# Kernel optimization log

Hardware: AMD Instinct MI355X
Metric: run time of the kernel (lower is better)

The kernel has to match this reference:

```python
import jax, jax.numpy as jnp
import numpy as np
from math import sqrt

H = 16
D_MODEL = 1024
D_K = D_MODEL // H
B, S = 2, 2048


def setup_inputs() -> dict:
    key = jax.random.key(0)
    ks = jax.random.split(key, 12)
    scale = 1.0 / sqrt(D_MODEL)
    inp = {
        "query": jax.random.normal(ks[0], (B, S, D_MODEL), jnp.float32),
        "key": jax.random.normal(ks[1], (B, S, D_MODEL), jnp.float32),
        "value": jax.random.normal(ks[2], (B, S, D_MODEL), jnp.float32),
        # causal mask [B, S, S]; module unsqueezes head dim itself
        "mask": jnp.broadcast_to(jnp.tril(jnp.ones((S, S), jnp.int32)), (B, S, S)),
        "Wq": jax.random.normal(ks[3], (D_MODEL, D_MODEL), jnp.float32) * scale,
        "bq": jnp.zeros((D_MODEL,), jnp.float32),
        "Wk": jax.random.normal(ks[4], (D_MODEL, D_MODEL), jnp.float32) * scale,
        "bk": jnp.zeros((D_MODEL,), jnp.float32),
        "Wv": jax.random.normal(ks[5], (D_MODEL, D_MODEL), jnp.float32) * scale,
        "bv": jnp.zeros((D_MODEL,), jnp.float32),
        "Wo": jax.random.normal(ks[6], (D_MODEL, D_MODEL), jnp.float32) * scale,
        "bo": jnp.zeros((D_MODEL,), jnp.float32),
    }
    return inp


def reference(query, key, value, mask, Wq, bq, Wk, bk, Wv, bv, Wo, bo):
    nb = query.shape[0]

    def proj(x, W, b):
        # nn.Linear: x @ W.T + b, then split heads -> [B, H, S, D_K]
        y = jnp.einsum('bsd,ed->bse', x, W) + b
        return y.reshape(nb, -1, H, D_K).transpose(0, 2, 1, 3)

    q = proj(query, Wq, bq)
    k = proj(key, Wk, bk)
    v = proj(value, Wv, bv)

    scores = jnp.einsum('bhqd,bhkd->bhqk', q, k) / sqrt(D_K)  # [B,H,S,S]
    scores = jnp.where(mask[:, None, :, :] == 0, -jnp.inf, scores)
    probs = jax.nn.softmax(scores, axis=-1)  # dropout in eval mode (identity)
    ctx = jnp.einsum('bhqk,bhkd->bhqd', probs, v)
    ctx = ctx.transpose(0, 2, 1, 3).reshape(nb, -1, H * D_K)
    return jnp.einsum('bsd,ed->bse', ctx, Wo) + bo
```

## Files before the change

kernel.cpp:

```cpp
#include <hip/hip_runtime.h>
#include <hip/hip_bf16.h>
#include <stdint.h>


#define H_ 16
#define DM 1024
#define DK_ 64
#define BB 2
#define SS 2048
#define PSTR 72

typedef __bf16 bf16x8 __attribute__((ext_vector_type(8)));
typedef __bf16 bf16x2_t __attribute__((ext_vector_type(2)));
typedef float f32x4 __attribute__((ext_vector_type(4)));

#define GLOAD_LDS16(g, l)                                            \
  __builtin_amdgcn_global_load_lds(                                  \
      (__attribute__((address_space(1))) void*)(g),                  \
      (__attribute__((address_space(3))) void*)(l), 16, 0, 0)

__device__ __forceinline__ unsigned short f2bf_u(float f) {
  unsigned int u = __float_as_uint(f);
  u += 0x7fffu + ((u >> 16) & 1u);
  return (unsigned short)(u >> 16);
}

__device__ __forceinline__ unsigned int pack_bf16(float a, float b) {
#if __has_builtin(__builtin_amdgcn_cvt_pk_bf16_f32)
  bf16x2_t v = __builtin_amdgcn_cvt_pk_bf16_f32(a, b);
  unsigned int u;
  __builtin_memcpy(&u, &v, 4);
  return u;
#else
  return (unsigned int)f2bf_u(a) | ((unsigned int)f2bf_u(b) << 16);
#endif
}

__device__ __forceinline__ float fexp2(float x) {
#if __has_builtin(__builtin_amdgcn_exp2f)
  return __builtin_amdgcn_exp2f(x);
#else
  return exp2f(x);
#endif
}

struct Cvt {
  const float* s[7];
  unsigned short* d[7];
  int n[7];
};

__global__ __launch_bounds__(256) void convert_kernel(Cvt c) {
  const int y = blockIdx.y;
  const float* __restrict__ src = c.s[y];
  unsigned short* __restrict__ dst = c.d[y];
  const int nv = c.n[y] >> 2;
  for (int i = blockIdx.x * 256 + threadIdx.x; i < nv; i += 1024 * 256) {
    float4 v = *(const float4*)(src + (size_t)i * 4);
    ushort4 o;
    o.x = f2bf_u(v.x); o.y = f2bf_u(v.y); o.z = f2bf_u(v.z); o.w = f2bf_u(v.w);
    *(ushort4*)(dst + (size_t)i * 4) = o;
  }
}

template <int TN>
__device__ __forceinline__ void gemm_dbuf(
    const unsigned short* __restrict__ A, const unsigned short* __restrict__ W,
    unsigned short* As, unsigned short* Bs, int m0, int n0,
    f32x4 (*acc)[TN / 32]) {
  constexpr int FW = TN / 32;
  const int tid = threadIdx.x;
  const int wave = tid >> 6, lane = tid & 63;
  const int lm = lane & 15, quad = lane >> 4;
  const int wm = (wave >> 1) * 64, wn = (wave & 1) * (16 * FW);
  const int srow = lane >> 2;
  const int scol = (lane & 3) * 8;

#pragma unroll
  for (int i = 0; i < 4; ++i)
#pragma unroll
    for (int j = 0; j < FW; ++j) {
      f32x4 z = {0.f, 0.f, 0.f, 0.f};
      acc[i][j] = z;
    }

#pragma unroll
  for (int cc = 0; cc < 2; ++cc) {
    int c = wave * 2 + cc;
    GLOAD_LDS16(A + (size_t)(m0 + c * 16 + srow) * DM + scol,
                As + c * 512 + lane * 8);
  }
  if (TN == 128) {
#pragma unroll
    for (int cc = 0; cc < 2; ++cc) {
      int c = wave * 2 + cc;
      GLOAD_LDS16(W + (size_t)(n0 + c * 16 + srow) * DM + scol,
                  Bs + c * 512 + lane * 8);
    }
  } else {
    GLOAD_LDS16(W + (size_t)(n0 + wave * 16 + srow) * DM + scol,
                Bs + wave * 512 + lane * 8);
  }

  for (int kt = 0; kt < DM / 32; ++kt) {
    __syncthreads();
    const int cur = kt & 1;
    const unsigned short* Ac = As + cur * (128 * 32);
    const unsigned short* Bc = Bs + cur * (TN * 32);
    if (kt + 1 < DM / 32) {
      unsigned short* An = As + (cur ^ 1) * (128 * 32);
      unsigned short* Bn = Bs + (cur ^ 1) * (TN * 32);
      const int kcol = (kt + 1) * 32 + scol;
#pragma unroll
      for (int cc = 0; cc < 2; ++cc) {
        int c = wave * 2 + cc;
        GLOAD_LDS16(A + (size_t)(m0 + c * 16 + srow) * DM + kcol,
                    An + c * 512 + lane * 8);
      }
      if (TN == 128) {
#pragma unroll
        for (int cc = 0; cc < 2; ++cc) {
          int c = wave * 2 + cc;
          GLOAD_LDS16(W + (size_t)(n0 + c * 16 + srow) * DM + kcol,
                      Bn + c * 512 + lane * 8);
        }
      } else {
        GLOAD_LDS16(W + (size_t)(n0 + wave * 16 + srow) * DM + kcol,
                    Bn + wave * 512 + lane * 8);
      }
    }
    bf16x8 af[4], bfr[FW];
#pragma unroll
    for (int i = 0; i < 4; ++i)
      af[i] = *(const bf16x8*)(Ac + (wm + i * 16 + lm) * 32 + quad * 8);
#pragma unroll
    for (int j = 0; j < FW; ++j)
      bfr[j] = *(const bf16x8*)(Bc + (wn + j * 16 + lm) * 32 + quad * 8);
#pragma unroll
    for (int i = 0; i < 4; ++i)
#pragma unroll
      for (int j = 0; j < FW; ++j)
        acc[i][j] = __builtin_amdgcn_mfma_f32_16x16x32_bf16(af[i], bfr[j],
                                                            acc[i][j], 0, 0, 0);
  }
}

__global__ __launch_bounds__(512, 2) void qkv_gemm(
    const unsigned short* Qi, const unsigned short* Ki, const unsigned short* Vi,
    const unsigned short* Wq, const unsigned short* Wk, const unsigned short* Wv,
    const float* bq, const float* bk, const float* bv,
    unsigned short* Qf, unsigned short* Kf, unsigned short* Vf) {
  __shared__ unsigned short As[2 * 2 * 16 * 512];
  __shared__ unsigned short Bs[2 * 2 * 16 * 512];
  const int p = blockIdx.x;
  const int c = p & 7, idx = p >> 3;
  const int x = idx & 3, yy = (idx >> 2) & 1, z = idx >> 3;
  const int y = c * 2 + yy;
  const int m0 = y * 256, n0 = x * 256;
  const unsigned short* A = z == 0 ? Qi : (z == 1 ? Ki : Vi);
  const unsigned short* W = z == 0 ? Wq : (z == 1 ? Wk : Wv);
  const float* bias = z == 0 ? bq : (z == 1 ? bk : bv);
  const float scale = z == 0 ? 0.125f : 1.0f;

  const int tid = threadIdx.x;
  const int wave = tid >> 6, lane = tid & 63;
  const int lm = lane & 15, quad = lane >> 4;
  const int wr = wave >> 2, wc = wave & 3;

  const int scs = 8 * ((lane & 3) ^ ((lane >> 3) & 3));
  const size_t asrc0 = (size_t)(m0 + wave * 16 + (lane >> 2)) * DM + scs;
  const size_t bsrc0 = (size_t)(n0 + wave * 16 + (lane >> 2)) * DM + scs;
  const int sdst = wave * 512 + lane * 8;

  const int rcol = (quad * 8) ^ (((lm >> 1) & 3) * 8);
  const int aoff = wr * 8 * 512 + lm * 32 + rcol;
  const int boff = wc * 4 * 512 + lm * 32 + rcol;

  f32x4 acc[8][4];
#pragma unroll
  for (int i = 0; i < 8; ++i)
#pragma unroll
    for (int j = 0; j < 4; ++j) {
      f32x4 zz = {0.f, 0.f, 0.f, 0.f};
      acc[i][j] = zz;
    }

  auto stA = [&](int buf, int kh, int kt) {
    const unsigned short* s = A + asrc0 + (size_t)kt * 64 + kh * 32;
    unsigned short* d = As + buf * 16384 + kh * 8192 + sdst;
    GLOAD_LDS16(s, d);
    GLOAD_LDS16(s + (size_t)128 * DM, d + 4096);
  };
  auto stB = [&](int buf, int kh, int kt) {
    const unsigned short* s = W + bsrc0 + (size_t)kt * 64 + kh * 32;
    unsigned short* d = Bs + buf * 16384 + kh * 8192 + sdst;
    GLOAD_LDS16(s, d);
    GLOAD_LDS16(s + (size_t)128 * DM, d + 4096);
  };

  stA(0, 0, 0); stB(0, 0, 0); stA(0, 1, 0); stB(0, 1, 0);
  stA(1, 0, 1); stB(1, 0, 1); stA(1, 1, 1);
  asm volatile("s_waitcnt vmcnt(6)" ::: "memory");
  __builtin_amdgcn_s_barrier();

#define BARR __builtin_amdgcn_s_barrier()
#define SCHB __builtin_amdgcn_sched_barrier(0)
#define MFMA8(AF, B0_, B1_, J0, J1)                                          \
  __builtin_amdgcn_s_setprio(1);                                             \
  _Pragma("unroll")                                                          \
  for (int i = 0; i < 8; ++i) {                                              \
    acc[i][J0] = __builtin_amdgcn_mfma_f32_16x16x32_bf16(AF[i], B0_,         \
                                                         acc[i][J0], 0, 0, 0); \
    acc[i][J1] = __builtin_amdgcn_mfma_f32_16x16x32_bf16(AF[i], B1_,         \
                                                         acc[i][J1], 0, 0, 0); \
  }                                                                          \
  __builtin_amdgcn_s_setprio(0)

#pragma unroll 2
  for (int t = 0; t < 14; ++t) {
    const int buf = t & 1;
    const unsigned short* Ab = As + buf * 16384;
    const unsigned short* Bb = Bs + buf * 16384;
    bf16x8 a0[8], b0[4];
#pragma unroll
    for (int i = 0; i < 8; ++i)
      a0[i] = *(const bf16x8*)(Ab + aoff + i * 512);
#pragma unroll
    for (int j = 0; j < 4; ++j)
      b0[j] = *(const bf16x8*)(Bb + boff + j * 512);
    stB(buf ^ 1, 1, t + 1);
    BARR; SCHB;
    MFMA8(a0, b0[0], b0[1], 0, 1);
    SCHB; BARR;
    stA(buf, 0, t + 2);
    BARR; SCHB;
    MFMA8(a0, b0[2], b0[3], 2, 3);
    SCHB; BARR;
    bf16x8 a1[8], b1[4];
#pragma unroll
    for (int i = 0; i < 8; ++i)
      a1[i] = *(const bf16x8*)(Ab + 8192 + aoff + i * 512);
#pragma unroll
    for (int j = 0; j < 4; ++j)
      b1[j] = *(const bf16x8*)(Bb + 8192 + boff + j * 512);
    stB(buf, 0, t + 2);
    BARR; SCHB;
    MFMA8(a1, b1[0], b1[1], 0, 1);
    SCHB; BARR;
    stA(buf, 1, t + 2);
    asm volatile("s_waitcnt vmcnt(6)" ::: "memory");
    BARR; SCHB;
    MFMA8(a1, b1[2], b1[3], 2, 3);
    SCHB; BARR;
  }

  stB(1, 1, 15);
  asm volatile("s_waitcnt vmcnt(0)" ::: "memory");
  __builtin_amdgcn_s_barrier();
#pragma unroll
  for (int tt = 0; tt < 2; ++tt) {
    const unsigned short* Ab = As + tt * 16384;
    const unsigned short* Bb = Bs + tt * 16384;
#pragma unroll
    for (int kh = 0; kh < 2; ++kh) {
      bf16x8 a2[8], b2[4];
#pragma unroll
      for (int i = 0; i < 8; ++i)
        a2[i] = *(const bf16x8*)(Ab + kh * 8192 + aoff + i * 512);
#pragma unroll
      for (int j = 0; j < 4; ++j)
        b2[j] = *(const bf16x8*)(Bb + kh * 8192 + boff + j * 512);
#pragma unroll
      for (int i = 0; i < 8; ++i)
#pragma unroll
        for (int j = 0; j < 4; ++j)
          acc[i][j] = __builtin_amdgcn_mfma_f32_16x16x32_bf16(
              a2[i], b2[j], acc[i][j], 0, 0, 0);
    }
  }
#undef MFMA8
#undef SCHB
#undef BARR

  if (z == 2) {
#pragma unroll
    for (int j = 0; j < 4; ++j) {
      int gn = n0 + wc * 64 + j * 16 + lm;
      float bv_ = bias[gn];
      int h2 = gn >> 6, dk = gn & 63;
      int a = dk >> 4, ln = dk & 15;
#pragma unroll
      for (int i = 0; i < 8; ++i) {
        int s0 = m0 + wr * 128 + i * 16 + quad * 4;
        int b2 = s0 >> 11, sl = s0 & 2047;
        int kt2 = sl >> 6, cc2 = (sl >> 5) & 1, qk = (sl >> 3) & 3, j0 = sl & 7;
        size_t base =
            ((size_t)(((b2 * 16 + h2) * 32 + kt2) * 4 + a) * 2 + cc2) * 512 +
            (qk * 16 + ln) * 8 + j0;
        uint2 w;
        w.x = pack_bf16(acc[i][j][0] + bv_, acc[i][j][1] + bv_);
        w.y = pack_bf16(acc[i][j][2] + bv_, acc[i][j][3] + bv_);
        *(uint2*)(Vf + base) = w;
      }
    }
  } else {
    unsigned short* out = z == 0 ? Qf : Kf;
#pragma unroll
    for (int j = 0; j < 4; ++j) {
      int gn = n0 + wc * 64 + j * 16 + lm;
      float bv_ = bias[gn];
      int h2 = gn >> 6, d64 = gn & 63;
      int cc2 = (d64 >> 5) & 1, qk = (d64 >> 3) & 3, jjq = d64 & 7;
#pragma unroll
      for (int i = 0; i < 8; ++i)
#pragma unroll
        for (int r = 0; r < 4; ++r) {
          int gm = m0 + wr * 128 + i * 16 + quad * 4 + r;
          int b2 = gm >> 11, sl = gm & 2047;
          size_t base =
              ((size_t)((b2 * 16 + h2) * 128 + (sl >> 4)) * 2 + cc2) * 512 +
              (qk * 16 + (sl & 15)) * 8 + jjq;
          out[base] = f2bf_u((acc[i][j][r] + bv_) * scale);
        }
    }
  }
}

__global__ __launch_bounds__(256) void o_gemm(
    const unsigned short* Ctx, const unsigned short* Wo, const float* bo,
    float* out) {
  __shared__ unsigned short As[2 * 128 * 32], Bs[2 * 64 * 32];
  const int p = blockIdx.x;
  const int c = p & 7, j0 = p >> 3;
  const int x = j0 & 15, yy = j0 >> 4;
  const int y = c * 4 + yy;
  const int m0 = y * 128, n0 = x * 64;
  f32x4 acc[4][2];
  gemm_dbuf<64>(Ctx, Wo, As, Bs, m0, n0, acc);
  const int lane = threadIdx.x & 63, wave = threadIdx.x >> 6;
  const int lm = lane & 15, quad = lane >> 4;
  const int wm = (wave >> 1) * 64, wn = (wave & 1) * 32;
#pragma unroll
  for (int j = 0; j < 2; ++j) {
    int gn = n0 + wn + j * 16 + lm;
    float bv_ = bo[gn];
#pragma unroll
    for (int i = 0; i < 4; ++i)
#pragma unroll
      for (int r = 0; r < 4; ++r) {
        int gm = m0 + wm + i * 16 + quad * 4 + r;
        out[(size_t)gm * DM + gn] = acc[i][j][r] + bv_;
      }
  }
}

__global__ __launch_bounds__(256, 4) void attn_kernel(
    const unsigned short* __restrict__ Qf, const unsigned short* __restrict__ Kf,
    const unsigned short* __restrict__ Vf, unsigned short* __restrict__ Ctx) {
  __shared__ unsigned short Ps[4][16 * PSTR];
  const int p = blockIdx.x;
  const int bh = p & 31, qb0 = p >> 5;
  const int qb = (bh & 1) ? (31 - qb0) : qb0;
  const int b = bh >> 4, h = bh & 15;
  const int tid = threadIdx.x, wave = tid >> 6, lane = tid & 63;
  const int lm = lane & 15, quad = lane >> 4;
  const float L2E = 1.4426950408889634f;

  const int qbase = qb * 64 + wave * 16;
  const int nkw = qb + 1;

  bf16x8 qf[2];
#pragma unroll
  for (int c = 0; c < 2; ++c)
    qf[c] = *(const bf16x8*)(Qf +
        ((size_t)(bh * 128 + (qbase >> 4)) * 2 + c) * 512 + lane * 8);

  const unsigned short* Kb = Kf + (size_t)bh * 256 * 512;
  const unsigned short* Vb = Vf + (size_t)bh * 256 * 512;
  unsigned short* Pw = Ps[wave];

  float lsum = 0.f;
  f32x4 oacc[4];
#pragma unroll
  for (int a = 0; a < 4; ++a) {
    f32x4 z = {0.f, 0.f, 0.f, 0.f};
    oacc[a] = z;
  }

  for (int kt = 0; kt < nkw; ++kt) {
    bf16x8 kf[4][2];
#pragma unroll
    for (int ik = 0; ik < 4; ++ik)
#pragma unroll
      for (int c = 0; c < 2; ++c)
        kf[ik][c] = *(const bf16x8*)(Kb +
            ((size_t)(kt * 4 + ik) * 2 + c) * 512 + lane * 8);
    f32x4 s[4];
#pragma unroll
    for (int ik = 0; ik < 4; ++ik) {
      f32x4 z = {0.f, 0.f, 0.f, 0.f};
      z = __builtin_amdgcn_mfma_f32_16x16x32_bf16(kf[ik][0], qf[0], z, 0, 0, 0);
      s[ik] = __builtin_amdgcn_mfma_f32_16x16x32_bf16(kf[ik][1], qf[1], z, 0, 0, 0);
    }
    if (kt == nkw - 1) {
#pragma unroll
      for (int ik = 0; ik < 4; ++ik)
#pragma unroll
        for (int r = 0; r < 4; ++r) {
          int kg = kt * 64 + ik * 16 + quad * 4 + r;
          int qg = qbase + lm;
          if (kg > qg) s[ik][r] = -1e30f;
        }
    }

    bf16x8 vf[4][2];
#pragma unroll
    for (int a = 0; a < 4; ++a)
#pragma unroll
      for (int c = 0; c < 2; ++c)
        vf[a][c] = *(const bf16x8*)(Vb +
            ((size_t)(kt * 8 + a * 2 + c)) * 512 + lane * 8);

#pragma unroll
    for (int ik = 0; ik < 4; ++ik) {
      float p0 = fexp2(s[ik][0] * L2E);
      float p1 = fexp2(s[ik][1] * L2E);
      float p2 = fexp2(s[ik][2] * L2E);
      float p3 = fexp2(s[ik][3] * L2E);
      lsum += (p0 + p1) + (p2 + p3);
      uint2 w;
      w.x = pack_bf16(p0, p1);
      w.y = pack_bf16(p2, p3);
      *(uint2*)(Pw + lm * PSTR + ik * 16 + quad * 4) = w;
    }

    bf16x8 pf[2];
#pragma unroll
    for (int c = 0; c < 2; ++c)
      pf[c] = *(const bf16x8*)(Pw + lm * PSTR + c * 32 + quad * 8);
#pragma unroll
    for (int a = 0; a < 4; ++a) {
      oacc[a] = __builtin_amdgcn_mfma_f32_16x16x32_bf16(pf[0], vf[a][0], oacc[a], 0, 0, 0);
      oacc[a] = __builtin_amdgcn_mfma_f32_16x16x32_bf16(pf[1], vf[a][1], oacc[a], 0, 0, 0);
    }
  }

  lsum += __shfl_xor(lsum, 16);
  lsum += __shfl_xor(lsum, 32);
#pragma unroll
  for (int r = 0; r < 4; ++r) {
    float inv = 1.0f / __shfl(lsum, quad * 4 + r);
    int qg = qbase + quad * 4 + r;
#pragma unroll
    for (int a = 0; a < 4; ++a)
      Ctx[(size_t)(b * SS + qg) * DM + h * DK_ + a * 16 + lm] =
          f2bf_u(oacc[a][r] * inv);
  }
}

extern "C" void kernel_launch(void* const* d_in, const int* in_sizes, int n_in,
                              void* d_out, int out_size, void* d_ws, size_t ws_size,
                              hipStream_t stream) {
  const float* q = (const float*)d_in[0];
  const float* k = (const float*)d_in[1];
  const float* v = (const float*)d_in[2];
  const float* Wq = (const float*)d_in[4];
  const float* bq = (const float*)d_in[5];
  const float* Wk = (const float*)d_in[6];
  const float* bk = (const float*)d_in[7];
  const float* Wv = (const float*)d_in[8];
  const float* bv = (const float*)d_in[9];
  const float* Wo = (const float*)d_in[10];
  const float* bo = (const float*)d_in[11];

  const size_t NX = (size_t)BB * SS * DM;
  const size_t NW = (size_t)DM * DM;
  unsigned short* ws = (unsigned short*)d_ws;
  unsigned short* Qi = ws;
  unsigned short* Ki = Qi + NX;
  unsigned short* Vi = Ki + NX;
  unsigned short* Wqb = Vi + NX;
  unsigned short* Wkb = Wqb + NW;
  unsigned short* Wvb = Wkb + NW;
  unsigned short* Wob = Wvb + NW;
  unsigned short* Qfr = Wob + NW;
  unsigned short* Kfr = Qfr + NX;
  unsigned short* Vfr = Kfr + NX;
  unsigned short* Ctx = Vfr + NX;

  Cvt c;
  c.s[0] = q; c.s[1] = k; c.s[2] = v; c.s[3] = Wq; c.s[4] = Wk; c.s[5] = Wv; c.s[6] = Wo;
  c.d[0] = Qi; c.d[1] = Ki; c.d[2] = Vi; c.d[3] = Wqb; c.d[4] = Wkb; c.d[5] = Wvb; c.d[6] = Wob;
  c.n[0] = c.n[1] = c.n[2] = (int)NX;
  c.n[3] = c.n[4] = c.n[5] = c.n[6] = (int)NW;

  convert_kernel<<<dim3(1024, 7), dim3(256), 0, stream>>>(c);
  qkv_gemm<<<dim3(192), dim3(512), 0, stream>>>(Qi, Ki, Vi, Wqb, Wkb, Wvb,
                                                bq, bk, bv, Qfr, Kfr, Vfr);
  attn_kernel<<<dim3(1024), dim3(256), 0, stream>>>(Qfr, Kfr, Vfr, Ctx);
  o_gemm<<<dim3(512), dim3(256), 0, stream>>>(Ctx, Wob, bo, (float*)d_out);
}
```

Measured before the change: 240.2 us.

## Pair causal query blocks per workgroup, double-buffer K/V, fold log2e into Q scale

The attention kernel now processes two query blocks per workgroup, a short one paired with a long one, so every block does the same causal work. This halves the grid. K and V fragments are register double-buffered so the next tile's loads are in flight while the current tile is computed. The row sums are computed with an MFMA against a ones vector instead of scalar adds and shuffles. The log2(e) factor is folded into the Q projection scale, which removes a multiply per exponential. In exchange, register pressure rises (launch bounds drop from 4 to 2 blocks per CU) and the row sum now uses bf16-rounded probabilities.

```diff
diff --git a/kernel.cpp b/kernel.cpp
--- a/kernel.cpp
+++ b/kernel.cpp
@@ -160,7 +160,7 @@
   const unsigned short* A = z == 0 ? Qi : (z == 1 ? Ki : Vi);
   const unsigned short* W = z == 0 ? Wq : (z == 1 ? Wk : Wv);
   const float* bias = z == 0 ? bq : (z == 1 ? bk : bv);
-  const float scale = z == 0 ? 0.125f : 1.0f;
+  const float scale = z == 0 ? 0.1803368801111204f : 1.0f;
 
   const int tid = threadIdx.x;
   const int wave = tid >> 6, lane = tid & 63;
@@ -354,107 +354,133 @@
   }
 }
 
-__global__ __launch_bounds__(256, 4) void attn_kernel(
+__global__ __launch_bounds__(256, 2) void attn_kernel(
     const unsigned short* __restrict__ Qf, const unsigned short* __restrict__ Kf,
     const unsigned short* __restrict__ Vf, unsigned short* __restrict__ Ctx) {
   __shared__ unsigned short Ps[4][16 * PSTR];
   const int p = blockIdx.x;
-  const int bh = p & 31, qb0 = p >> 5;
-  const int qb = (bh & 1) ? (31 - qb0) : qb0;
+  const int bh = p & 31, pr = p >> 5;
   const int b = bh >> 4, h = bh & 15;
   const int tid = threadIdx.x, wave = tid >> 6, lane = tid & 63;
   const int lm = lane & 15, quad = lane >> 4;
-  const float L2E = 1.4426950408889634f;
-
-  const int qbase = qb * 64 + wave * 16;
-  const int nkw = qb + 1;
-
-  bf16x8 qf[2];
-#pragma unroll
-  for (int c = 0; c < 2; ++c)
-    qf[c] = *(const bf16x8*)(Qf +
-        ((size_t)(bh * 128 + (qbase >> 4)) * 2 + c) * 512 + lane * 8);
 
   const unsigned short* Kb = Kf + (size_t)bh * 256 * 512;
   const unsigned short* Vb = Vf + (size_t)bh * 256 * 512;
   unsigned short* Pw = Ps[wave];
 
-  float lsum = 0.f;
-  f32x4 oacc[4];
-#pragma unroll
-  for (int a = 0; a < 4; ++a) {
-    f32x4 z = {0.f, 0.f, 0.f, 0.f};
-    oacc[a] = z;
-  }
-
-  for (int kt = 0; kt < nkw; ++kt) {
-    bf16x8 kf[4][2];
+  bf16x8 onesf;
+  {
+    unsigned short ob[8] = {0x3F80, 0x3F80, 0x3F80, 0x3F80,
+                            0x3F80, 0x3F80, 0x3F80, 0x3F80};
+    __builtin_memcpy(&onesf, ob, 16);
+  }
+
+  auto loadK = [&](bf16x8 (&kf)[4][2], int kt) {
 #pragma unroll
     for (int ik = 0; ik < 4; ++ik)
 #pragma unroll
       for (int c = 0; c < 2; ++c)
         kf[ik][c] = *(const bf16x8*)(Kb +
             ((size_t)(kt * 4 + ik) * 2 + c) * 512 + lane * 8);
-    f32x4 s[4];
-#pragma unroll
-    for (int ik = 0; ik < 4; ++ik) {
-      f32x4 z = {0.f, 0.f, 0.f, 0.f};
-      z = __builtin_amdgcn_mfma_f32_16x16x32_bf16(kf[ik][0], qf[0], z, 0, 0, 0);
-      s[ik] = __builtin_amdgcn_mfma_f32_16x16x32_bf16(kf[ik][1], qf[1], z, 0, 0, 0);
-    }
-    if (kt == nkw - 1) {
-#pragma unroll
-      for (int ik = 0; ik < 4; ++ik)
-#pragma unroll
-        for (int r = 0; r < 4; ++r) {
-          int kg = kt * 64 + ik * 16 + quad * 4 + r;
-          int qg = qbase + lm;
-          if (kg > qg) s[ik][r] = -1e30f;
-        }
-    }
-
-    bf16x8 vf[4][2];
+  };
+  auto loadV = [&](bf16x8 (&vf)[4][2], int kt) {
 #pragma unroll
     for (int a = 0; a < 4; ++a)
 #pragma unroll
       for (int c = 0; c < 2; ++c)
         vf[a][c] = *(const bf16x8*)(Vb +
             ((size_t)(kt * 8 + a * 2 + c)) * 512 + lane * 8);
-
-#pragma unroll
-    for (int ik = 0; ik < 4; ++ik) {
-      float p0 = fexp2(s[ik][0] * L2E);
-      float p1 = fexp2(s[ik][1] * L2E);
-      float p2 = fexp2(s[ik][2] * L2E);
-      float p3 = fexp2(s[ik][3] * L2E);
-      lsum += (p0 + p1) + (p2 + p3);
-      uint2 w;
-      w.x = pack_bf16(p0, p1);
-      w.y = pack_bf16(p2, p3);
-      *(uint2*)(Pw + lm * PSTR + ik * 16 + quad * 4) = w;
-    }
-
-    bf16x8 pf[2];
+  };
+
+  for (int pass = 0; pass < 2; ++pass) {
+    const int qb = pass ? 31 - pr : pr;
+    const int qbase = qb * 64 + wave * 16;
+    const int nkw = qb + 1;
+
+    bf16x8 qf[2];
 #pragma unroll
     for (int c = 0; c < 2; ++c)
-      pf[c] = *(const bf16x8*)(Pw + lm * PSTR + c * 32 + quad * 8);
+      qf[c] = *(const bf16x8*)(Qf +
+          ((size_t)(bh * 128 + (qbase >> 4)) * 2 + c) * 512 + lane * 8);
+
+    f32x4 oacc[4];
 #pragma unroll
     for (int a = 0; a < 4; ++a) {
-      oacc[a] = __builtin_amdgcn_mfma_f32_16x16x32_bf16(pf[0], vf[a][0], oacc[a], 0, 0, 0);
-      oacc[a] = __builtin_amdgcn_mfma_f32_16x16x32_bf16(pf[1], vf[a][1], oacc[a], 0, 0, 0);
-    }
-  }
-
-  lsum += __shfl_xor(lsum, 16);
-  lsum += __shfl_xor(lsum, 32);
-#pragma unroll
-  for (int r = 0; r < 4; ++r) {
-    float inv = 1.0f / __shfl(lsum, quad * 4 + r);
-    int qg = qbase + quad * 4 + r;
-#pragma unroll
-    for (int a = 0; a < 4; ++a)
-      Ctx[(size_t)(b * SS + qg) * DM + h * DK_ + a * 16 + lm] =
-          f2bf_u(oacc[a][r] * inv);
+      f32x4 z = {0.f, 0.f, 0.f, 0.f};
+      oacc[a] = z;
+    }
+    f32x4 lacc = {0.f, 0.f, 0.f, 0.f};
+
+    auto compute = [&](bf16x8 (&kf)[4][2], bf16x8 (&vf)[4][2], int kt,
+                       bool last) {
+      f32x4 s[4];
+#pragma unroll
+      for (int ik = 0; ik < 4; ++ik) {
+        f32x4 zz = {0.f, 0.f, 0.f, 0.f};
+        zz = __builtin_amdgcn_mfma_f32_16x16x32_bf16(kf[ik][0], qf[0], zz,
+                                                     0, 0, 0);
+        s[ik] = __builtin_amdgcn_mfma_f32_16x16x32_bf16(kf[ik][1], qf[1], zz,
+                                                        0, 0, 0);
+      }
+      if (last) {
+#pragma unroll
+        for (int ik = 0; ik < 4; ++ik)
+#pragma unroll
+          for (int r = 0; r < 4; ++r) {
+            int kg = kt * 64 + ik * 16 + quad * 4 + r;
+            int qg = qbase + lm;
+            if (kg > qg) s[ik][r] = -1e30f;
+          }
+      }
+#pragma unroll
+      for (int ik = 0; ik < 4; ++ik) {
+        float p0 = fexp2(s[ik][0]);
+        float p1 = fexp2(s[ik][1]);
+        float p2 = fexp2(s[ik][2]);
+        float p3 = fexp2(s[ik][3]);
+        uint2 w;
+        w.x = pack_bf16(p0, p1);
+        w.y = pack_bf16(p2, p3);
+        *(uint2*)(Pw + lm * PSTR + ik * 16 + quad * 4) = w;
+      }
+      bf16x8 pf[2];
+#pragma unroll
+      for (int c = 0; c < 2; ++c)
+        pf[c] = *(const bf16x8*)(Pw + lm * PSTR + c * 32 + quad * 8);
+#pragma unroll
+      for (int a = 0; a < 4; ++a) {
+        oacc[a] = __builtin_amdgcn_mfma_f32_16x16x32_bf16(pf[0], vf[a][0],
+                                                          oacc[a], 0, 0, 0);
+        oacc[a] = __builtin_amdgcn_mfma_f32_16x16x32_bf16(pf[1], vf[a][1],
+                                                          oacc[a], 0, 0, 0);
+      }
+      lacc = __builtin_amdgcn_mfma_f32_16x16x32_bf16(pf[0], onesf, lacc,
+                                                     0, 0, 0);
+      lacc = __builtin_amdgcn_mfma_f32_16x16x32_bf16(pf[1], onesf, lacc,
+                                                     0, 0, 0);
+    };
+
+    bf16x8 kA[4][2], vA[4][2], kB[4][2], vB[4][2];
+    loadK(kA, 0);
+    loadV(vA, 0);
+    for (int kt = 0; kt < nkw; kt += 2) {
+      if (kt + 1 < nkw) { loadK(kB, kt + 1); loadV(vB, kt + 1); }
+      compute(kA, vA, kt, kt == nkw - 1);
+      if (kt + 1 < nkw) {
+        if (kt + 2 < nkw) { loadK(kA, kt + 2); loadV(vA, kt + 2); }
+        compute(kB, vB, kt + 1, kt + 1 == nkw - 1);
+      }
+    }
+
+#pragma unroll
+    for (int r = 0; r < 4; ++r) {
+      float inv = 1.0f / lacc[r];
+      int qg = qbase + quad * 4 + r;
+#pragma unroll
+      for (int a = 0; a < 4; ++a)
+        Ctx[(size_t)(b * SS + qg) * DM + h * DK_ + a * 16 + lm] =
+            f2bf_u(oacc[a][r] * inv);
+    }
   }
 }
 
@@ -497,6 +523,6 @@
   convert_kernel<<<dim3(1024, 7), dim3(256), 0, stream>>>(c);
   qkv_gemm<<<dim3(192), dim3(512), 0, stream>>>(Qi, Ki, Vi, Wqb, Wkb, Wvb,
                                                 bq, bk, bv, Qfr, Kfr, Vfr);
-  attn_kernel<<<dim3(1024), dim3(256), 0, stream>>>(Qfr, Kfr, Vfr, Ctx);
+  attn_kernel<<<dim3(512), dim3(256), 0, stream>>>(Qfr, Kfr, Vfr, Ctx);
   o_gemm<<<dim3(512), dim3(256), 0, stream>>>(Ctx, Wob, bo, (float*)d_out);
 }
```

Measured after the change: 233.8 us. -2.7%, faster.
